# Optimization experiments

Measured on AMD Instinct MI355X. Metric: run time of the kernel, lower is better.

The kernel has to match this reference:

```python
import jax, jax.numpy as jnp
import numpy as np

DEPTH, HEADS, DIM, DH = 6, 3, 3, 128
INNER = HEADS * DH            # 384
M = int(DH * np.log(DH))      # 620 random features (performer_pytorch default)
FF = 4 * DIM                  # 12
EPS = 1e-4


def setup_inputs() -> dict:
    key = jax.random.key(0)
    ks = jax.random.split(key, 12)
    B, N = 8, 4096
    s = 0.1
    return {
        "x": jax.random.normal(ks[0], (B, N, DIM), jnp.float32),
        "Wq": jax.random.normal(ks[1], (DEPTH, DIM, INNER), jnp.float32) * s,
        "Wk": jax.random.normal(ks[2], (DEPTH, DIM, INNER), jnp.float32) * s,
        "Wv": jax.random.normal(ks[3], (DEPTH, DIM, INNER), jnp.float32) * s,
        "Wo": jax.random.normal(ks[4], (DEPTH, INNER, DIM), jnp.float32) * s,
        "bo": jnp.zeros((DEPTH, DIM), jnp.float32),
        "ln1_g": jnp.ones((DEPTH, DIM), jnp.float32),
        "ln1_b": jnp.zeros((DEPTH, DIM), jnp.float32),
        "W1": jax.random.normal(ks[5], (DEPTH, DIM, FF), jnp.float32) * s,
        "b1": jnp.zeros((DEPTH, FF), jnp.float32),
        "W2": jax.random.normal(ks[6], (DEPTH, FF, DIM), jnp.float32) * s,
        "b2": jnp.zeros((DEPTH, DIM), jnp.float32),
        "ln2_g": jnp.ones((DEPTH, DIM), jnp.float32),
        "ln2_b": jnp.zeros((DEPTH, DIM), jnp.float32),
        "proj": jax.random.normal(ks[7], (DEPTH, M, DH), jnp.float32),
        "dec_w": jax.random.normal(ks[8], (DIM, 1), jnp.float32) * s,
        "dec_b": jnp.zeros((1,), jnp.float32),
    }


def layernorm(x, g, b):
    mu = x.mean(-1, keepdims=True)
    var = ((x - mu) ** 2).mean(-1, keepdims=True)
    return (x - mu) * jax.lax.rsqrt(var + 1e-5) * g + b


def softmax_kernel(data, proj, is_query):
    # data: [b,h,n,dh], proj: [m,dh] -> positive random features [b,h,n,m]
    dn = DH ** -0.25                    # data normalizer 1/sqrt(sqrt(d))
    ratio = M ** -0.5
    dd = jnp.einsum('bhnd,md->bhnm', data * dn, proj)
    diag = 0.5 * (dn ** 2) * (data ** 2).sum(-1, keepdims=True)  # [b,h,n,1]
    if is_query:
        mx = jnp.max(dd, axis=-1, keepdims=True)
    else:
        mx = jnp.max(dd, axis=(-1, -2), keepdims=True)
    return ratio * (jnp.exp(dd - diag - mx) + EPS)


def favor_attention(x, Wq, Wk, Wv, Wo, bo, proj):
    b, n, _ = x.shape
    split = lambda t: t.reshape(b, n, HEADS, DH).transpose(0, 2, 1, 3)
    q, k, v = split(x @ Wq), split(x @ Wk), split(x @ Wv)   # [b,h,n,dh]
    qp = softmax_kernel(q, proj, True)    # [b,h,n,m]
    kp = softmax_kernel(k, proj, False)
    k_sum = kp.sum(axis=2)                                   # [b,h,m]
    d_inv = 1.0 / jnp.einsum('bhnm,bhm->bhn', qp, k_sum)
    ctx = jnp.einsum('bhnm,bhnd->bhmd', kp, v)               # [b,h,m,dh]
    out = jnp.einsum('bhnm,bhmd,bhn->bhnd', qp, ctx, d_inv)
    out = out.transpose(0, 2, 1, 3).reshape(b, n, INNER)
    return out @ Wo + bo


def reference(x, Wq, Wk, Wv, Wo, bo, ln1_g, ln1_b, W1, b1, W2, b2, ln2_g, ln2_b, proj, dec_w, dec_b):
    for i in range(DEPTH):
        h = layernorm(x, ln1_g[i], ln1_b[i])
        x = x + favor_attention(h, Wq[i], Wk[i], Wv[i], Wo[i], bo[i], proj[i])
        h = layernorm(x, ln2_g[i], ln2_b[i])
        x = x + (jax.nn.gelu(h @ W1[i] + b1[i], approximate=False) @ W2[i] + b2[i])
    return jax.nn.sigmoid(x @ dec_w + dec_b)
```

## Files before the change

kernel.cpp:

```cpp
#include <hip/hip_runtime.h>
#include <math.h>

#define B_ 8
#define N_ 4096
#define H_ 3
#define DH_ 128
#define INNER_ 384
#define M_ 620
#define MP_ 640
#define DEPTH_ 6
#define BH_ 24

static constexpr float DN_ = 0.29730177875068026f;
static constexpr float RATIO_ = 0.04016096644512494f;
static constexpr float EPS_ = 1e-4f;

typedef __attribute__((ext_vector_type(8))) short short8;
typedef __attribute__((ext_vector_type(4))) float f32x4;

__device__ __forceinline__ short f2bf(float f) {
  union { float f; unsigned u; } x; x.f = f;
  unsigned r = x.u + 0x7FFF + ((x.u >> 16) & 1);
  return (short)(r >> 16);
}
__device__ __forceinline__ float bf2f(short s) {
  union { unsigned u; float f; } x; x.u = ((unsigned)(unsigned short)s) << 16;
  return x.f;
}
__device__ __forceinline__ float4 ldg4(const float* p) { return *(const float4*)p; }

__device__ __forceinline__ unsigned cvtpk(float lo, float hi) {
  unsigned r;
  asm("v_cvt_pk_bf16_f32 %0, %1, %2" : "=v"(r) : "v"(lo), "v"(hi));
  return r;
}

__device__ __forceinline__ void gl2lds(const void* g, void* l) {
  __builtin_amdgcn_global_load_lds(
      (const __attribute__((address_space(1))) void*)g,
      (__attribute__((address_space(3))) void*)l, 16, 0, 0);
}

__device__ __forceinline__ void stage_t256(const char* gbase, char* lds, int w, int l) {
  int row = w * 4 + (l >> 4);
  int col = ((l & 15) * 16) ^ ((row & 7) << 4);
  char* lp = lds + __builtin_amdgcn_readfirstlane(w << 10);
  gl2lds(gbase + row * 256 + col, lp);
}

__device__ __forceinline__ void stage_t64(const char* gbase, size_t growb, char* lds,
                                          int w, int l) {
  int d = w * 16 + (l >> 2);
  int swl = ((((l >> 2) ^ (l >> 4)) & 3) << 4);
  int col = ((l & 3) * 16) ^ swl;
  char* lp = lds + __builtin_amdgcn_readfirstlane(w << 10);
  gl2lds(gbase + (size_t)d * growb + col, lp);
}

__global__ void k_copy(const float* __restrict__ s, float* __restrict__ d, int n) {
  int i = blockIdx.x * 256 + threadIdx.x;
  if (i < n) d[i] = s[i];
}

__global__ void k_projcvt(const float* __restrict__ proj, short* __restrict__ pb) {
  int i = blockIdx.x * 256 + threadIdx.x;
  if (i >= DEPTH_ * MP_ * DH_) return;
  int l = i / (MP_ * DH_);
  int rem = i - l * (MP_ * DH_);
  int m = rem >> 7, d = rem & 127;
  pb[i] = (m < M_) ? f2bf(proj[((size_t)l * M_ + m) * DH_ + d]) : (short)0;
}

__global__ __launch_bounds__(384) void k_ln_qkv(
    const float* __restrict__ x, const float* __restrict__ Wq,
    const float* __restrict__ Wk, const float* __restrict__ Wv,
    const float* __restrict__ g1, const float* __restrict__ b1,
    short* __restrict__ qb, short* __restrict__ kb, short* __restrict__ vtp) {
  __shared__ float xs[96];
  int c = threadIdx.x;
  int token0 = blockIdx.x * 32;
  int b = token0 >> 12, n0 = token0 & 4095;
  if (c < 96) xs[c] = x[(size_t)token0 * 3 + c];
  float wq0 = Wq[c], wq1 = Wq[INNER_ + c], wq2 = Wq[2 * INNER_ + c];
  float wk0 = Wk[c], wk1 = Wk[INNER_ + c], wk2 = Wk[2 * INNER_ + c];
  float wv0 = Wv[c], wv1 = Wv[INNER_ + c], wv2 = Wv[2 * INNER_ + c];
  float G0 = g1[0], G1 = g1[1], G2 = g1[2];
  float B0 = b1[0], B1 = b1[1], B2 = b1[2];
  int hh = c >> 7, dh = c & 127;
  size_t rowbase = ((size_t)(b * H_ + hh) * N_ + n0) * DH_ + dh;
  __syncthreads();
  short8 v8[4];
#pragma unroll
  for (int tt = 0; tt < 32; ++tt) {
    float x0 = xs[tt * 3], x1 = xs[tt * 3 + 1], x2 = xs[tt * 3 + 2];
    float mu = (x0 + x1 + x2) * (1.f / 3.f);
    float d0 = x0 - mu, d1 = x1 - mu, d2 = x2 - mu;
    float rs = rsqrtf((d0 * d0 + d1 * d1 + d2 * d2) * (1.f / 3.f) + 1e-5f);
    float h0 = d0 * rs * G0 + B0;
    float h1 = d1 * rs * G1 + B1;
    float h2 = d2 * rs * G2 + B2;
    qb[rowbase + (size_t)tt * DH_] = f2bf((h0 * wq0 + h1 * wq1 + h2 * wq2) * DN_);
    kb[rowbase + (size_t)tt * DH_] = f2bf((h0 * wk0 + h1 * wk1 + h2 * wk2) * DN_);
    const int p = ((tt >> 2) & 3) * 8 + ((tt >> 4) & 1) * 4 + (tt & 3);
    v8[p >> 3][p & 7] = f2bf(h0 * wv0 + h1 * wv1 + h2 * wv2);
  }
  short* dst = vtp + ((size_t)(b * H_ + hh) * DH_ + dh) * N_ + n0;
  *(short8*)dst = v8[0];
  *(short8*)(dst + 8) = v8[1];
  *(short8*)(dst + 16) = v8[2];
  *(short8*)(dst + 24) = v8[3];
}

__global__ __launch_bounds__(512) void k_kmax(
    const short* __restrict__ kb, const short* __restrict__ pb,
    float* __restrict__ blkmax, float* __restrict__ diag_k) {
  int nt = blockIdx.x, bh = blockIdx.y;
  __shared__ __align__(16) char Pj[2][8192];
  __shared__ float red[8];
  int t = threadIdx.x, w = t >> 6, l = t & 63, lr = l & 15, lg = l >> 4;
  const short* kr = kb + ((size_t)bh * N_ + nt * 128 + w * 16 + lr) * DH_ + lg * 8;
  short8 afr[4];
#pragma unroll
  for (int ks = 0; ks < 4; ++ks) afr[ks] = *(const short8*)(kr + ks * 32);
  {
    float s2 = 0.f;
#pragma unroll
    for (int ks = 0; ks < 4; ++ks)
#pragma unroll
      for (int j = 0; j < 8; ++j) {
        float v = bf2f(afr[ks][j]);
        s2 = fmaf(v, v, s2);
      }
    s2 += __shfl_xor(s2, 16);
    s2 += __shfl_xor(s2, 32);
    if (l < 16) diag_k[(size_t)bh * N_ + nt * 128 + w * 16 + lr] = 0.5f * s2;
  }
  stage_t256((const char*)pb, Pj[0], w, l);
  __syncthreads();
  float vmax = -INFINITY;
  int xk = (lr & 7) << 4;
  for (int mc = 0; mc < 20; ++mc) {
    int cur = mc & 1;
    if (mc < 19) stage_t256((const char*)(pb + (size_t)(mc + 1) * 32 * DH_),
                            Pj[cur ^ 1], w, l);
#pragma unroll
    for (int ms = 0; ms < 2; ++ms) {
      int m = mc * 32 + ms * 16 + lr;
      f32x4 acc = {0.f, 0.f, 0.f, 0.f};
#pragma unroll
      for (int ks = 0; ks < 4; ++ks)
        acc = __builtin_amdgcn_mfma_f32_16x16x32_bf16(
            afr[ks],
            *(const short8*)(Pj[cur] + (ms * 16 + lr) * 256 +
                             ((lg * 16 + ks * 64) ^ xk)),
            acc, 0, 0, 0);
      if (m < M_)
        vmax = fmaxf(vmax, fmaxf(fmaxf(acc[0], acc[1]), fmaxf(acc[2], acc[3])));
    }
    __syncthreads();
  }
#pragma unroll
  for (int off = 1; off < 64; off <<= 1) vmax = fmaxf(vmax, __shfl_xor(vmax, off));
  if (l == 0) red[w] = vmax;
  __syncthreads();
  if (t == 0) {
    float m = red[0];
#pragma unroll
    for (int i = 1; i < 8; ++i) m = fmaxf(m, red[i]);
    blkmax[bh * 32 + nt] = m;
  }
}

__global__ __launch_bounds__(512) void k_kp_ctx(
    const short* __restrict__ kb, const short* __restrict__ vtp,
    const short* __restrict__ pb, const float* __restrict__ diag_k,
    const float* __restrict__ blkmax,
    float* __restrict__ Cpart, float* __restrict__ spart) {
  int ns = blockIdx.x, mt = blockIdx.y, bh = blockIdx.z;
  __shared__ __align__(16) char Ks[2][8192];
  __shared__ __align__(16) char Vts[2][8192];
  __shared__ float diag_s[1024];
  __shared__ float mxs_s;
  int t = threadIdx.x, w = t >> 6, l = t & 63, lr = l & 15, lg = l >> 4;
  {
    const float* dbase = diag_k + (size_t)bh * N_ + ns * 1024;
#pragma unroll
    for (int i = 0; i < 2; ++i) diag_s[t + i * 512] = dbase[t + i * 512];
  }
  if (t < 32) {
    float m = blkmax[bh * 32 + t];
#pragma unroll
    for (int off = 16; off; off >>= 1) m = fmaxf(m, __shfl_xor(m, off));
    if (t == 0) mxs_s = m;
  }
  int m0 = mt * 128 + w * 16;
  short8 bfr[4];
  {
    const short* pr = pb + (size_t)(m0 + lr) * DH_ + lg * 8;
#pragma unroll
    for (int ks = 0; ks < 4; ++ks) bfr[ks] = *(const short8*)(pr + ks * 32);
  }
  const char* kgb = (const char*)(kb + ((size_t)bh * N_ + ns * 1024) * DH_);
  const char* vgb = (const char*)(vtp + (size_t)bh * DH_ * N_ + ns * 1024);
  stage_t256(kgb, Ks[0], w, l);
  stage_t64(vgb, (size_t)N_ * 2, Vts[0], w, l);
  __syncthreads();
  float mxv = mxs_s;
  f32x4 cacc[8];
#pragma unroll
  for (int db = 0; db < 8; ++db) cacc[db] = (f32x4){0.f, 0.f, 0.f, 0.f};
  float ksacc = 0.f;
  int xk = (lr & 7) << 4;
  int xv = ((lr ^ (lr >> 2)) & 3) << 4;
  for (int ch = 0; ch < 32; ++ch) {
    int cur = ch & 1;
    if (ch < 31) {
      stage_t256(kgb + (size_t)(ch + 1) * 32 * 256, Ks[cur ^ 1], w, l);
      stage_t64(vgb + (size_t)(ch + 1) * 64, (size_t)N_ * 2, Vts[cur ^ 1], w, l);
    }
    int n0 = ch * 32;
    float ev[8];
    __builtin_amdgcn_s_setprio(1);
#pragma unroll
    for (int nsub = 0; nsub < 2; ++nsub) {
      f32x4 acc = {0.f, 0.f, 0.f, 0.f};
#pragma unroll
      for (int ks = 0; ks < 4; ++ks)
        acc = __builtin_amdgcn_mfma_f32_16x16x32_bf16(
            *(const short8*)(Ks[cur] + (nsub * 16 + lr) * 256 +
                             ((lg * 16 + ks * 64) ^ xk)),
            bfr[ks], acc, 0, 0, 0);
#pragma unroll
      for (int rg = 0; rg < 4; ++rg) {
        float e = __expf(acc[rg] - diag_s[n0 + nsub * 16 + 4 * lg + rg] - mxv);
        ev[nsub * 4 + rg] = e;
        ksacc += e;
      }
    }
    __builtin_amdgcn_s_setprio(0);
    union { short8 s8; unsigned u[4]; } ea;
#pragma unroll
    for (int i = 0; i < 4; ++i) ea.u[i] = cvtpk(ev[2 * i], ev[2 * i + 1]);
    __builtin_amdgcn_s_setprio(1);
#pragma unroll
    for (int db = 0; db < 8; ++db)
      cacc[db] = __builtin_amdgcn_mfma_f32_16x16x32_bf16(
          ea.s8, *(const short8*)(Vts[cur] + (db * 16 + lr) * 64 + ((lg * 16) ^ xv)),
          cacc[db], 0, 0, 0);
    __builtin_amdgcn_s_setprio(0);
    __syncthreads();
  }
  float* Cp = Cpart + ((size_t)ns * BH_ + bh) * MP_ * DH_;
#pragma unroll
  for (int db = 0; db < 8; ++db) {
    int d = db * 16 + lr;
#pragma unroll
    for (int rg = 0; rg < 4; ++rg)
      Cp[(size_t)(m0 + 4 * lg + rg) * DH_ + d] = cacc[db][rg];
  }
  ksacc += __shfl_down(ksacc, 32);
  ksacc += __shfl_down(ksacc, 16);
  if (l < 16) spart[((size_t)ns * BH_ + bh) * MP_ + m0 + l] = ksacc;
}

__global__ __launch_bounds__(256) void k_vsum(
    const short* __restrict__ vtp, float* __restrict__ vsp) {
  int d = blockIdx.x, bh = blockIdx.y, t = threadIdx.x;
  const short8* row = (const short8*)(vtp + ((size_t)bh * DH_ + d) * N_);
  short8 a = row[t * 2], b2 = row[t * 2 + 1];
  float s = 0.f;
#pragma unroll
  for (int j = 0; j < 8; ++j) s += bf2f(a[j]) + bf2f(b2[j]);
  __shared__ float red[256];
  red[t] = s;
  __syncthreads();
  for (int st = 128; st; st >>= 1) {
    if (t < st) red[t] += red[t + st];
    __syncthreads();
  }
  if (t == 0) vsp[bh * DH_ + d] = red[0];
}

__global__ __launch_bounds__(256) void k_fin_ctx(
    const float* __restrict__ Cpart, const float* __restrict__ vsp,
    short* __restrict__ ctxtp, float* __restrict__ cspart) {
  int mt = blockIdx.x, bh = blockIdx.y;
  __shared__ float vsv[128];
  __shared__ short tile[128][40];
  int t = threadIdx.x;
  if (t < 128) vsv[t] = vsp[bh * DH_ + t] * EPS_;
  __syncthreads();
  int r = t >> 3, seg = t & 7;
  int d0 = seg * 16;
  int m = mt * 32 + r;
  int p = ((r >> 2) & 3) * 8 + ((r >> 4) & 1) * 4 + (r & 3);
  const size_t ph = (size_t)BH_ * MP_ * DH_;
  const float* c0 = Cpart + (size_t)bh * MP_ * DH_ + (size_t)m * DH_ + d0;
  if (m < M_) {
#pragma unroll
    for (int j4 = 0; j4 < 4; ++j4) {
      float4 a = ldg4(c0 + j4 * 4);
      float4 b = ldg4(c0 + ph + j4 * 4);
      float4 c = ldg4(c0 + 2 * ph + j4 * 4);
      float4 e = ldg4(c0 + 3 * ph + j4 * 4);
      float vals[4] = {a.x + b.x + c.x + e.x, a.y + b.y + c.y + e.y,
                       a.z + b.z + c.z + e.z, a.w + b.w + c.w + e.w};
#pragma unroll
      for (int j = 0; j < 4; ++j) {
        int d = d0 + j4 * 4 + j;
        tile[d][p] = f2bf(RATIO_ * (vals[j] + vsv[d]));
      }
    }
  } else {
#pragma unroll
    for (int j = 0; j < 16; ++j) tile[d0 + j][p] = 0;
  }
  __syncthreads();
  int d = t >> 1, half = t & 1;
  short* dst = ctxtp + ((size_t)bh * DH_ + d) * MP_ + mt * 32 + half * 16;
  short8 s0 = *(const short8*)&tile[d][half * 16];
  short8 s1 = *(const short8*)&tile[d][half * 16 + 8];
  *(short8*)dst = s0;
  *(short8*)(dst + 8) = s1;
  float cs = 0.f;
#pragma unroll
  for (int j = 0; j < 8; ++j) cs += bf2f(s0[j]) + bf2f(s1[j]);
  cs += __shfl_xor(cs, 1);
  if (half == 0) cspart[((size_t)bh * 20 + mt) * DH_ + d] = cs;
}

__global__ __launch_bounds__(128) void k_fin2(
    const float* __restrict__ cspart, const float* __restrict__ spart,
    float* __restrict__ ctxsum, short* __restrict__ ksum_pb,
    float* __restrict__ ksumtot) {
  int bh = blockIdx.x, d = threadIdx.x;
  float s = 0.f;
#pragma unroll
  for (int mt = 0; mt < 20; ++mt) s += cspart[((size_t)bh * 20 + mt) * DH_ + d];
  ctxsum[bh * DH_ + d] = s;
  __shared__ float red[128];
  float kt = 0.f;
  for (int m = d; m < MP_; m += 128) {
    float ks = 0.f;
    if (m < M_) {
      size_t o = (size_t)bh * MP_ + m;
      size_t sh = (size_t)BH_ * MP_;
      ks = RATIO_ * (spart[o] + spart[o + sh] + spart[o + 2 * sh] + spart[o + 3 * sh] +
                     EPS_ * (float)N_);
    }
    int r = m & 31;
    int p = ((r >> 2) & 3) * 8 + ((r >> 4) & 1) * 4 + (r & 3);
    ksum_pb[(size_t)bh * MP_ + (m & ~31) + p] = f2bf(ks);
    kt += ks;
  }
  red[d] = kt;
  __syncthreads();
  for (int st = 64; st > 0; st >>= 1) {
    if (d < st) red[d] += red[d + st];
    __syncthreads();
  }
  if (d == 0) ksumtot[bh] = red[0];
}

__global__ __launch_bounds__(512) void k_q_attn(
    const short* __restrict__ qb, const short* __restrict__ pb,
    const short* __restrict__ ctxtp, const short* __restrict__ ksum_pb,
    const float* __restrict__ ctxsum, const float* __restrict__ ksumtot,
    float* __restrict__ o) {
  int nt = blockIdx.x, bh = blockIdx.y;
  __shared__ __align__(16) char Pj[2][8192];
  __shared__ __align__(16) char Ct[2][8192];
  __shared__ __align__(16) short kslp[MP_];
  int t = threadIdx.x, w = t >> 6, l = t & 63, lr = l & 15, lg = l >> 4;
  if (t < MP_ / 8)
    ((short8*)kslp)[t] = ((const short8*)(ksum_pb + (size_t)bh * MP_))[t];
  const short* qr = qb + ((size_t)bh * N_ + nt * 128 + w * 16 + lr) * DH_ + lg * 8;
  short8 qfr[4];
#pragma unroll
  for (int ks = 0; ks < 4; ++ks) qfr[ks] = *(const short8*)(qr + ks * 32);
  float dq;
  {
    float s2 = 0.f;
#pragma unroll
    for (int ks = 0; ks < 4; ++ks)
#pragma unroll
      for (int j = 0; j < 8; ++j) {
        float v = bf2f(qfr[ks][j]);
        s2 = fmaf(v, v, s2);
      }
    s2 += __shfl_xor(s2, 16);
    s2 += __shfl_xor(s2, 32);
    dq = 0.5f * s2;
  }
  const char* cgb = (const char*)(ctxtp + (size_t)bh * DH_ * MP_);
  stage_t256((const char*)pb, Pj[0], w, l);
  stage_t64(cgb, (size_t)MP_ * 2, Ct[0], w, l);
  __syncthreads();
  f32x4 cacc[8];
#pragma unroll
  for (int db = 0; db < 8; ++db) cacc[db] = (f32x4){0.f, 0.f, 0.f, 0.f};
  f32x4 dacc = {0.f, 0.f, 0.f, 0.f};
  float om = -INFINITY;
  int xk = (lr & 7) << 4;
  int xv = ((lr ^ (lr >> 2)) & 3) << 4;
  for (int mc = 0; mc < 20; ++mc) {
    int cur = mc & 1;
    if (mc < 19) {
      stage_t256((const char*)(pb + (size_t)(mc + 1) * 32 * DH_), Pj[cur ^ 1], w, l);
      stage_t64(cgb + (size_t)(mc + 1) * 64, (size_t)MP_ * 2, Ct[cur ^ 1], w, l);
    }
    int m0 = mc * 32;
    f32x4 qk[2];
    __builtin_amdgcn_s_setprio(1);
#pragma unroll
    for (int ms = 0; ms < 2; ++ms) {
      f32x4 acc = {0.f, 0.f, 0.f, 0.f};
#pragma unroll
      for (int ks = 0; ks < 4; ++ks)
        acc = __builtin_amdgcn_mfma_f32_16x16x32_bf16(
            *(const short8*)(Pj[cur] + (ms * 16 + lr) * 256 +
                             ((lg * 16 + ks * 64) ^ xk)),
            qfr[ks], acc, 0, 0, 0);
      qk[ms] = acc;
    }
    __builtin_amdgcn_s_setprio(0);
    float cm = -INFINITY;
#pragma unroll
    for (int ms = 0; ms < 2; ++ms)
#pragma unroll
      for (int rg = 0; rg < 4; ++rg) {
        int mg = m0 + ms * 16 + 4 * lg + rg;
        if (mg < M_) cm = fmaxf(cm, qk[ms][rg]);
      }
    cm = fmaxf(cm, __shfl_xor(cm, 16));
    cm = fmaxf(cm, __shfl_xor(cm, 32));
    if (__any(cm > om)) {
      float nm = fmaxf(om, cm);
      float sc = __expf(om - nm);
      om = nm;
      float scr[4];
#pragma unroll
      for (int rg = 0; rg < 4; ++rg) scr[rg] = __shfl(sc, 4 * lg + rg);
#pragma unroll
      for (int rg = 0; rg < 4; ++rg) dacc[rg] *= scr[rg];
#pragma unroll
      for (int db = 0; db < 8; ++db)
#pragma unroll
        for (int rg = 0; rg < 4; ++rg) cacc[db][rg] *= scr[rg];
    }
    float dqm = dq + om;
    float ev[8];
#pragma unroll
    for (int ms = 0; ms < 2; ++ms)
#pragma unroll
      for (int rg = 0; rg < 4; ++rg)
        ev[ms * 4 + rg] = __expf(qk[ms][rg] - dqm);
    union { short8 s8; unsigned u[4]; } ea;
#pragma unroll
    for (int i = 0; i < 4; ++i) ea.u[i] = cvtpk(ev[2 * i], ev[2 * i + 1]);
    __builtin_amdgcn_s_setprio(1);
    dacc = __builtin_amdgcn_mfma_f32_16x16x32_bf16(
        ea.s8, *(const short8*)&kslp[m0 + lg * 8], dacc, 0, 0, 0);
#pragma unroll
    for (int db = 0; db < 8; ++db)
      cacc[db] = __builtin_amdgcn_mfma_f32_16x16x32_bf16(
          ea.s8, *(const short8*)(Ct[cur] + (db * 16 + lr) * 64 + ((lg * 16) ^ xv)),
          cacc[db], 0, 0, 0);
    __builtin_amdgcn_s_setprio(0);
    __syncthreads();
  }
  float kst = ksumtot[bh];
  float dinv[4];
#pragma unroll
  for (int rg = 0; rg < 4; ++rg)
    dinv[rg] = 1.f / (RATIO_ * (dacc[rg] + EPS_ * kst));
  float* ob = o + ((size_t)bh * N_ + nt * 128 + w * 16) * DH_;
#pragma unroll
  for (int db = 0; db < 8; ++db) {
    int d = db * 16 + lr;
    float cs = ctxsum[bh * DH_ + d] * EPS_;
#pragma unroll
    for (int rg = 0; rg < 4; ++rg)
      ob[(size_t)(4 * lg + rg) * DH_ + d] = RATIO_ * (cacc[db][rg] + cs) * dinv[rg];
  }
}

__global__ __launch_bounds__(256) void k_wo_ffn(
    const float* __restrict__ attn, const float* __restrict__ Wo,
    const float* __restrict__ bo, const float* __restrict__ g2,
    const float* __restrict__ be2, const float* __restrict__ W1,
    const float* __restrict__ bf1, const float* __restrict__ W2,
    const float* __restrict__ bf2, float* __restrict__ x) {
  __shared__ float wols[INNER_ * 3];
  __shared__ float bos[3];
  __shared__ float acc3[4][8][3];
  int t = threadIdx.x;
  for (int i = t; i < INNER_ * 3; i += 256) wols[i] = Wo[i];
  if (t < 3) bos[t] = bo[t];
  __syncthreads();
  int w = t >> 6, l = t & 63;
  int base = (blockIdx.x * 4 + w) * 8;
#pragma unroll
  for (int tt = 0; tt < 8; ++tt) {
    int token = base + tt;
    int b = token >> 12, n = token & 4095;
    float p0 = 0.f, p1 = 0.f, p2 = 0.f;
#pragma unroll
    for (int s = 0; s < 6; ++s) {
      int inner = l + 64 * s;
      int h = inner >> 7, dh = inner & 127;
      float a = attn[(((size_t)(b * H_ + h)) * N_ + n) * DH_ + dh];
      p0 = fmaf(a, wols[inner * 3 + 0], p0);
      p1 = fmaf(a, wols[inner * 3 + 1], p1);
      p2 = fmaf(a, wols[inner * 3 + 2], p2);
    }
#pragma unroll
    for (int off = 32; off; off >>= 1) {
      p0 += __shfl_down(p0, off);
      p1 += __shfl_down(p1, off);
      p2 += __shfl_down(p2, off);
    }
    if (l == 0) {
      acc3[w][tt][0] = p0 + bos[0];
      acc3[w][tt][1] = p1 + bos[1];
      acc3[w][tt][2] = p2 + bos[2];
    }
  }
  __syncthreads();
  if (l < 8) {
    int token = base + l;
    float x0 = x[(size_t)token * 3 + 0] + acc3[w][l][0];
    float x1 = x[(size_t)token * 3 + 1] + acc3[w][l][1];
    float x2 = x[(size_t)token * 3 + 2] + acc3[w][l][2];
    float mu = (x0 + x1 + x2) * (1.f / 3.f);
    float d0 = x0 - mu, d1 = x1 - mu, d2 = x2 - mu;
    float rs = rsqrtf((d0 * d0 + d1 * d1 + d2 * d2) * (1.f / 3.f) + 1e-5f);
    float h0 = d0 * rs * g2[0] + be2[0];
    float h1 = d1 * rs * g2[1] + be2[1];
    float h2 = d2 * rs * g2[2] + be2[2];
    float y0 = x0 + bf2[0], y1 = x1 + bf2[1], y2 = x2 + bf2[2];
#pragma unroll
    for (int tt = 0; tt < 12; ++tt) {
      float f = h0 * W1[tt] + h1 * W1[12 + tt] + h2 * W1[24 + tt] + bf1[tt];
      float g = 0.5f * f * (1.f + erff(f * 0.70710678118654752f));
      y0 += g * W2[tt * 3 + 0];
      y1 += g * W2[tt * 3 + 1];
      y2 += g * W2[tt * 3 + 2];
    }
    x[(size_t)token * 3 + 0] = y0;
    x[(size_t)token * 3 + 1] = y1;
    x[(size_t)token * 3 + 2] = y2;
  }
}

__global__ void k_decode(const float* __restrict__ x, const float* __restrict__ dw,
                         const float* __restrict__ db, float* __restrict__ out) {
  int t = blockIdx.x * 256 + threadIdx.x;
  if (t < B_ * N_) {
    float l = x[(size_t)t * 3 + 0] * dw[0] + x[(size_t)t * 3 + 1] * dw[1] +
              x[(size_t)t * 3 + 2] * dw[2] + db[0];
    out[t] = 1.f / (1.f + expf(-l));
  }
}

extern "C" void kernel_launch(void* const* d_in, const int* in_sizes, int n_in,
                              void* d_out, int out_size, void* d_ws, size_t ws_size,
                              hipStream_t stream) {
  const float* x_in = (const float*)d_in[0];
  const float* Wq = (const float*)d_in[1];
  const float* Wk = (const float*)d_in[2];
  const float* Wv = (const float*)d_in[3];
  const float* Wo = (const float*)d_in[4];
  const float* bo = (const float*)d_in[5];
  const float* ln1g = (const float*)d_in[6];
  const float* ln1b = (const float*)d_in[7];
  const float* W1 = (const float*)d_in[8];
  const float* b1 = (const float*)d_in[9];
  const float* W2 = (const float*)d_in[10];
  const float* b2 = (const float*)d_in[11];
  const float* ln2g = (const float*)d_in[12];
  const float* ln2b = (const float*)d_in[13];
  const float* proj = (const float*)d_in[14];
  const float* dec_w = (const float*)d_in[15];
  const float* dec_b = (const float*)d_in[16];

  const size_t XB = (size_t)B_ * N_ * 3;
  const size_t QKV = (size_t)BH_ * N_ * DH_;
  const size_t CTX = (size_t)BH_ * MP_ * DH_;
  const size_t SS = (size_t)BH_ * MP_;

  char* p = (char*)d_ws;
  auto alloc = [&](size_t bytes) {
    char* r = p;
    p += (bytes + 255) & ~(size_t)255;
    return r;
  };
  float* xbuf = (float*)alloc(XB * 4);
  short* qb = (short*)alloc(QKV * 2);
  short* kb = (short*)alloc(QKV * 2);
  float* diag_k = (float*)alloc((size_t)BH_ * N_ * 4);
  short* pb = (short*)alloc((size_t)DEPTH_ * MP_ * DH_ * 2);
  short* vtp = (short*)alloc(QKV * 2);
  short* ctxtp = (short*)alloc(CTX * 2);
  float* o = (float*)alloc(QKV * 4);
  float* Cpart = o;
  float* spart = (float*)alloc(4 * SS * 4);
  float* cspart = (float*)alloc((size_t)BH_ * 20 * DH_ * 4);
  short* ksum_pb = (short*)alloc(SS * 2);
  float* vsp = (float*)alloc((size_t)BH_ * DH_ * 4);
  float* ctxsum = (float*)alloc((size_t)BH_ * DH_ * 4);
  float* ksumtot = (float*)alloc(BH_ * 4);
  float* blkmax = (float*)alloc((size_t)BH_ * 32 * 4);

  k_copy<<<(XB + 255) / 256, 256, 0, stream>>>(x_in, xbuf, (int)XB);
  k_projcvt<<<(DEPTH_ * MP_ * DH_ + 255) / 256, 256, 0, stream>>>(proj, pb);

  for (int i = 0; i < DEPTH_; ++i) {
    const short* pbL = pb + (size_t)i * MP_ * DH_;
    k_ln_qkv<<<B_ * N_ / 32, 384, 0, stream>>>(xbuf, Wq + (size_t)i * 3 * INNER_,
                                               Wk + (size_t)i * 3 * INNER_,
                                               Wv + (size_t)i * 3 * INNER_,
                                               ln1g + i * 3, ln1b + i * 3,
                                               qb, kb, vtp);
    k_kmax<<<dim3(32, BH_), 512, 0, stream>>>(kb, pbL, blkmax, diag_k);
    k_kp_ctx<<<dim3(4, 5, BH_), 512, 0, stream>>>(kb, vtp, pbL, diag_k, blkmax,
                                                  Cpart, spart);
    k_vsum<<<dim3(DH_, BH_), 256, 0, stream>>>(vtp, vsp);
    k_fin_ctx<<<dim3(20, BH_), 256, 0, stream>>>(Cpart, vsp, ctxtp, cspart);
    k_fin2<<<BH_, 128, 0, stream>>>(cspart, spart, ctxsum, ksum_pb, ksumtot);
    k_q_attn<<<dim3(32, BH_), 512, 0, stream>>>(qb, pbL, ctxtp, ksum_pb,
                                                ctxsum, ksumtot, o);
    k_wo_ffn<<<B_ * N_ / 32, 256, 0, stream>>>(o, Wo + (size_t)i * INNER_ * 3,
                                               bo + i * 3, ln2g + i * 3, ln2b + i * 3,
                                               W1 + (size_t)i * 36, b1 + (size_t)i * 12,
                                               W2 + (size_t)i * 36, b2 + i * 3, xbuf);
  }
  k_decode<<<(B_ * N_ + 255) / 256, 256, 0, stream>>>(xbuf, dec_w, dec_b, (float*)d_out);
}
```

Measured before the change: 1.083 ms.

## Replace separate key-max pass with online running-max rescaling in kp_ctx

Result: no change. 1.075 ms, median of 2 (-0.7%).

```diff
diff --git a/kernel.cpp b/kernel.cpp
--- a/kernel.cpp
+++ b/kernel.cpp
@@ -111,87 +111,41 @@
   *(short8*)(dst + 24) = v8[3];
 }
 
-__global__ __launch_bounds__(512) void k_kmax(
-    const short* __restrict__ kb, const short* __restrict__ pb,
-    float* __restrict__ blkmax, float* __restrict__ diag_k) {
+__global__ __launch_bounds__(256) void k_diag(const short* __restrict__ kb,
+                                              float* __restrict__ diag_k) {
   int nt = blockIdx.x, bh = blockIdx.y;
-  __shared__ __align__(16) char Pj[2][8192];
-  __shared__ float red[8];
-  int t = threadIdx.x, w = t >> 6, l = t & 63, lr = l & 15, lg = l >> 4;
-  const short* kr = kb + ((size_t)bh * N_ + nt * 128 + w * 16 + lr) * DH_ + lg * 8;
-  short8 afr[4];
-#pragma unroll
-  for (int ks = 0; ks < 4; ++ks) afr[ks] = *(const short8*)(kr + ks * 32);
-  {
-    float s2 = 0.f;
-#pragma unroll
-    for (int ks = 0; ks < 4; ++ks)
-#pragma unroll
-      for (int j = 0; j < 8; ++j) {
-        float v = bf2f(afr[ks][j]);
-        s2 = fmaf(v, v, s2);
-      }
-    s2 += __shfl_xor(s2, 16);
-    s2 += __shfl_xor(s2, 32);
-    if (l < 16) diag_k[(size_t)bh * N_ + nt * 128 + w * 16 + lr] = 0.5f * s2;
-  }
-  stage_t256((const char*)pb, Pj[0], w, l);
-  __syncthreads();
-  float vmax = -INFINITY;
-  int xk = (lr & 7) << 4;
-  for (int mc = 0; mc < 20; ++mc) {
-    int cur = mc & 1;
-    if (mc < 19) stage_t256((const char*)(pb + (size_t)(mc + 1) * 32 * DH_),
-                            Pj[cur ^ 1], w, l);
-#pragma unroll
-    for (int ms = 0; ms < 2; ++ms) {
-      int m = mc * 32 + ms * 16 + lr;
-      f32x4 acc = {0.f, 0.f, 0.f, 0.f};
-#pragma unroll
-      for (int ks = 0; ks < 4; ++ks)
-        acc = __builtin_amdgcn_mfma_f32_16x16x32_bf16(
-            afr[ks],
-            *(const short8*)(Pj[cur] + (ms * 16 + lr) * 256 +
-                             ((lg * 16 + ks * 64) ^ xk)),
-            acc, 0, 0, 0);
-      if (m < M_)
-        vmax = fmaxf(vmax, fmaxf(fmaxf(acc[0], acc[1]), fmaxf(acc[2], acc[3])));
-    }
-    __syncthreads();
-  }
-#pragma unroll
-  for (int off = 1; off < 64; off <<= 1) vmax = fmaxf(vmax, __shfl_xor(vmax, off));
-  if (l == 0) red[w] = vmax;
-  __syncthreads();
-  if (t == 0) {
-    float m = red[0];
-#pragma unroll
-    for (int i = 1; i < 8; ++i) m = fmaxf(m, red[i]);
-    blkmax[bh * 32 + nt] = m;
-  }
+  int t = threadIdx.x;
+  int n = t >> 3, seg = t & 7;
+  const short* src = kb + ((size_t)bh * N_ + nt * 32 + n) * DH_ + seg * 16;
+  short8 a = *(const short8*)src;
+  short8 b2 = *(const short8*)(src + 8);
+  float s = 0.f;
+#pragma unroll
+  for (int j = 0; j < 8; ++j) {
+    float va = bf2f(a[j]), vb = bf2f(b2[j]);
+    s = fmaf(va, va, s);
+    s = fmaf(vb, vb, s);
+  }
+  s += __shfl_down(s, 4);
+  s += __shfl_down(s, 2);
+  s += __shfl_down(s, 1);
+  if (seg == 0) diag_k[(size_t)bh * N_ + nt * 32 + n] = 0.5f * s;
 }
 
 __global__ __launch_bounds__(512) void k_kp_ctx(
     const short* __restrict__ kb, const short* __restrict__ vtp,
     const short* __restrict__ pb, const float* __restrict__ diag_k,
-    const float* __restrict__ blkmax,
-    float* __restrict__ Cpart, float* __restrict__ spart) {
+    float* __restrict__ Cpart, float* __restrict__ spart,
+    float* __restrict__ bmx) {
   int ns = blockIdx.x, mt = blockIdx.y, bh = blockIdx.z;
   __shared__ __align__(16) char Ks[2][8192];
   __shared__ __align__(16) char Vts[2][8192];
   __shared__ float diag_s[1024];
-  __shared__ float mxs_s;
   int t = threadIdx.x, w = t >> 6, l = t & 63, lr = l & 15, lg = l >> 4;
   {
     const float* dbase = diag_k + (size_t)bh * N_ + ns * 1024;
 #pragma unroll
     for (int i = 0; i < 2; ++i) diag_s[t + i * 512] = dbase[t + i * 512];
-  }
-  if (t < 32) {
-    float m = blkmax[bh * 32 + t];
-#pragma unroll
-    for (int off = 16; off; off >>= 1) m = fmaxf(m, __shfl_xor(m, off));
-    if (t == 0) mxs_s = m;
   }
   int m0 = mt * 128 + w * 16;
   short8 bfr[4];
@@ -205,11 +159,12 @@
   stage_t256(kgb, Ks[0], w, l);
   stage_t64(vgb, (size_t)N_ * 2, Vts[0], w, l);
   __syncthreads();
-  float mxv = mxs_s;
   f32x4 cacc[8];
 #pragma unroll
   for (int db = 0; db < 8; ++db) cacc[db] = (f32x4){0.f, 0.f, 0.f, 0.f};
   float ksacc = 0.f;
+  float bm = -INFINITY;
+  const bool mv = (m0 + lr) < M_;
   int xk = (lr & 7) << 4;
   int xv = ((lr ^ (lr >> 2)) & 3) << 4;
   for (int ch = 0; ch < 32; ++ch) {
@@ -219,7 +174,7 @@
       stage_t64(vgb + (size_t)(ch + 1) * 64, (size_t)N_ * 2, Vts[cur ^ 1], w, l);
     }
     int n0 = ch * 32;
-    float ev[8];
+    f32x4 dd[2];
     __builtin_amdgcn_s_setprio(1);
 #pragma unroll
     for (int nsub = 0; nsub < 2; ++nsub) {
@@ -230,14 +185,36 @@
             *(const short8*)(Ks[cur] + (nsub * 16 + lr) * 256 +
                              ((lg * 16 + ks * 64) ^ xk)),
             bfr[ks], acc, 0, 0, 0);
+      dd[nsub] = acc;
+    }
+    __builtin_amdgcn_s_setprio(0);
+    float cm = -INFINITY;
+    if (mv) {
+#pragma unroll
+      for (int nsub = 0; nsub < 2; ++nsub)
+#pragma unroll
+        for (int rg = 0; rg < 4; ++rg) cm = fmaxf(cm, dd[nsub][rg]);
+    }
+#pragma unroll
+    for (int off = 1; off < 64; off <<= 1) cm = fmaxf(cm, __shfl_xor(cm, off));
+    if (cm > bm) {
+      float sc = __expf(bm - cm);
+      bm = cm;
+      ksacc *= sc;
+#pragma unroll
+      for (int db = 0; db < 8; ++db)
+#pragma unroll
+        for (int rg = 0; rg < 4; ++rg) cacc[db][rg] *= sc;
+    }
+    float ev[8];
+#pragma unroll
+    for (int nsub = 0; nsub < 2; ++nsub)
 #pragma unroll
       for (int rg = 0; rg < 4; ++rg) {
-        float e = __expf(acc[rg] - diag_s[n0 + nsub * 16 + 4 * lg + rg] - mxv);
+        float e = __expf(dd[nsub][rg] - diag_s[n0 + nsub * 16 + 4 * lg + rg] - bm);
         ev[nsub * 4 + rg] = e;
         ksacc += e;
       }
-    }
-    __builtin_amdgcn_s_setprio(0);
     union { short8 s8; unsigned u[4]; } ea;
 #pragma unroll
     for (int i = 0; i < 4; ++i) ea.u[i] = cvtpk(ev[2 * i], ev[2 * i + 1]);
@@ -261,6 +238,23 @@
   ksacc += __shfl_down(ksacc, 32);
   ksacc += __shfl_down(ksacc, 16);
   if (l < 16) spart[((size_t)ns * BH_ + bh) * MP_ + m0 + l] = ksacc;
+  if (l == 0) bmx[((size_t)ns * BH_ + bh) * 40 + mt * 8 + w] = bm;
+}
+
+__global__ __launch_bounds__(256) void k_gmax(const float* __restrict__ bmx,
+                                              float* __restrict__ mxk) {
+  int bh = blockIdx.x, t = threadIdx.x;
+  float v = -INFINITY;
+  if (t < 160) {
+    int ns = t / 40, g = t - ns * 40;
+    v = bmx[((size_t)ns * BH_ + bh) * 40 + g];
+  }
+#pragma unroll
+  for (int off = 32; off; off >>= 1) v = fmaxf(v, __shfl_xor(v, off));
+  __shared__ float red[4];
+  if ((t & 63) == 0) red[t >> 6] = v;
+  __syncthreads();
+  if (t == 0) mxk[bh] = fmaxf(fmaxf(red[0], red[1]), fmaxf(red[2], red[3]));
 }
 
 __global__ __launch_bounds__(256) void k_vsum(
@@ -283,6 +277,7 @@
 
 __global__ __launch_bounds__(256) void k_fin_ctx(
     const float* __restrict__ Cpart, const float* __restrict__ vsp,
+    const float* __restrict__ bmx, const float* __restrict__ mxk,
     short* __restrict__ ctxtp, float* __restrict__ cspart) {
   int mt = blockIdx.x, bh = blockIdx.y;
   __shared__ float vsv[128];
@@ -297,14 +292,22 @@
   const size_t ph = (size_t)BH_ * MP_ * DH_;
   const float* c0 = Cpart + (size_t)bh * MP_ * DH_ + (size_t)m * DH_ + d0;
   if (m < M_) {
+    float mxg = mxk[bh];
+    int g = m >> 4;
+    float sc0 = __expf(bmx[((size_t)0 * BH_ + bh) * 40 + g] - mxg);
+    float sc1 = __expf(bmx[((size_t)1 * BH_ + bh) * 40 + g] - mxg);
+    float sc2 = __expf(bmx[((size_t)2 * BH_ + bh) * 40 + g] - mxg);
+    float sc3 = __expf(bmx[((size_t)3 * BH_ + bh) * 40 + g] - mxg);
 #pragma unroll
     for (int j4 = 0; j4 < 4; ++j4) {
       float4 a = ldg4(c0 + j4 * 4);
       float4 b = ldg4(c0 + ph + j4 * 4);
       float4 c = ldg4(c0 + 2 * ph + j4 * 4);
       float4 e = ldg4(c0 + 3 * ph + j4 * 4);
-      float vals[4] = {a.x + b.x + c.x + e.x, a.y + b.y + c.y + e.y,
-                       a.z + b.z + c.z + e.z, a.w + b.w + c.w + e.w};
+      float vals[4] = {sc0 * a.x + sc1 * b.x + sc2 * c.x + sc3 * e.x,
+                       sc0 * a.y + sc1 * b.y + sc2 * c.y + sc3 * e.y,
+                       sc0 * a.z + sc1 * b.z + sc2 * c.z + sc3 * e.z,
+                       sc0 * a.w + sc1 * b.w + sc2 * c.w + sc3 * e.w};
 #pragma unroll
       for (int j = 0; j < 4; ++j) {
         int d = d0 + j4 * 4 + j;
@@ -331,6 +334,7 @@
 
 __global__ __launch_bounds__(128) void k_fin2(
     const float* __restrict__ cspart, const float* __restrict__ spart,
+    const float* __restrict__ bmx, const float* __restrict__ mxk,
     float* __restrict__ ctxsum, short* __restrict__ ksum_pb,
     float* __restrict__ ksumtot) {
   int bh = blockIdx.x, d = threadIdx.x;
@@ -338,6 +342,7 @@
 #pragma unroll
   for (int mt = 0; mt < 20; ++mt) s += cspart[((size_t)bh * 20 + mt) * DH_ + d];
   ctxsum[bh * DH_ + d] = s;
+  float mxg = mxk[bh];
   __shared__ float red[128];
   float kt = 0.f;
   for (int m = d; m < MP_; m += 128) {
@@ -345,8 +350,13 @@
     if (m < M_) {
       size_t o = (size_t)bh * MP_ + m;
       size_t sh = (size_t)BH_ * MP_;
-      ks = RATIO_ * (spart[o] + spart[o + sh] + spart[o + 2 * sh] + spart[o + 3 * sh] +
-                     EPS_ * (float)N_);
+      int g = m >> 4;
+      float s0 = __expf(bmx[((size_t)0 * BH_ + bh) * 40 + g] - mxg);
+      float s1 = __expf(bmx[((size_t)1 * BH_ + bh) * 40 + g] - mxg);
+      float s2 = __expf(bmx[((size_t)2 * BH_ + bh) * 40 + g] - mxg);
+      float s3 = __expf(bmx[((size_t)3 * BH_ + bh) * 40 + g] - mxg);
+      ks = RATIO_ * (s0 * spart[o] + s1 * spart[o + sh] + s2 * spart[o + 2 * sh] +
+                     s3 * spart[o + 3 * sh] + EPS_ * (float)N_);
     }
     int r = m & 31;
     int p = ((r >> 2) & 3) * 8 + ((r >> 4) & 1) * 4 + (r & 3);
@@ -610,7 +620,8 @@
   float* vsp = (float*)alloc((size_t)BH_ * DH_ * 4);
   float* ctxsum = (float*)alloc((size_t)BH_ * DH_ * 4);
   float* ksumtot = (float*)alloc(BH_ * 4);
-  float* blkmax = (float*)alloc((size_t)BH_ * 32 * 4);
+  float* bmx = (float*)alloc((size_t)4 * BH_ * 40 * 4);
+  float* mxk = (float*)alloc(BH_ * 4);
 
   k_copy<<<(XB + 255) / 256, 256, 0, stream>>>(x_in, xbuf, (int)XB);
   k_projcvt<<<(DEPTH_ * MP_ * DH_ + 255) / 256, 256, 0, stream>>>(proj, pb);
@@ -622,12 +633,15 @@
                                                Wv + (size_t)i * 3 * INNER_,
                                                ln1g + i * 3, ln1b + i * 3,
                                                qb, kb, vtp);
-    k_kmax<<<dim3(32, BH_), 512, 0, stream>>>(kb, pbL, blkmax, diag_k);
-    k_kp_ctx<<<dim3(4, 5, BH_), 512, 0, stream>>>(kb, vtp, pbL, diag_k, blkmax,
-                                                  Cpart, spart);
+    k_diag<<<dim3(N_ / 32, BH_), 256, 0, stream>>>(kb, diag_k);
+    k_kp_ctx<<<dim3(4, 5, BH_), 512, 0, stream>>>(kb, vtp, pbL, diag_k,
+                                                  Cpart, spart, bmx);
     k_vsum<<<dim3(DH_, BH_), 256, 0, stream>>>(vtp, vsp);
-    k_fin_ctx<<<dim3(20, BH_), 256, 0, stream>>>(Cpart, vsp, ctxtp, cspart);
-    k_fin2<<<BH_, 128, 0, stream>>>(cspart, spart, ctxsum, ksum_pb, ksumtot);
+    k_gmax<<<BH_, 256, 0, stream>>>(bmx, mxk);
+    k_fin_ctx<<<dim3(20, BH_), 256, 0, stream>>>(Cpart, vsp, bmx, mxk,
+                                                 ctxtp, cspart);
+    k_fin2<<<BH_, 128, 0, stream>>>(cspart, spart, bmx, mxk,
+                                    ctxsum, ksum_pb, ksumtot);
     k_q_attn<<<dim3(32, BH_), 512, 0, stream>>>(qb, pbL, ctxtp, ksum_pb,
                                                 ctxsum, ksumtot, o);
     k_wo_ffn<<<B_ * N_ / 32, 256, 0, stream>>>(o, Wo + (size_t)i * INNER_ * 3,
```
